# Kernel optimization log

Measured on AMD Instinct MI355X. Metric: run time of the kernel, lower is better.

Reference implementation:

```python
import jax, jax.numpy as jnp
import numpy as np

NUM_LOW, NUM_HIGH, DIM = 8192, 1024, 2048
EPS = 1e-10


def sparsemax(z):
    # z: [..., K]; Martins & Astudillo sparsemax along last axis.
    K = z.shape[-1]
    z_sorted = jnp.flip(jnp.sort(z, axis=-1), axis=-1)          # descending
    z_cum = jnp.cumsum(z_sorted, axis=-1)
    k = jnp.arange(1, K + 1, dtype=z.dtype)
    support = (1.0 + k * z_sorted) > z_cum                       # bool [..., K]
    k_sup = jnp.sum(support, axis=-1, keepdims=True)             # int [..., 1]
    tau = (jnp.take_along_axis(z_cum, k_sup - 1, axis=-1) - 1.0) / k_sup.astype(z.dtype)
    return jnp.maximum(z - tau, 0.0)


def normalize_rows(x, eps=EPS):
    return x / (jnp.sum(x, axis=1, keepdims=True) + eps)


def setup_inputs() -> dict:
    key = jax.random.key(0)
    k1, k2, k3, k4 = jax.random.split(key, 4)

    def xavier(k, shape):
        bound = float(np.sqrt(6.0 / (shape[0] + shape[1])))
        return jax.random.uniform(k, shape, jnp.float32, -bound, bound)

    return {
        "low_w": xavier(k1, (NUM_LOW, DIM)),    # low Concepts parameter
        "high_w": xavier(k2, (NUM_HIGH, DIM)),  # high Concepts parameter
        "Wq": xavier(k3, (DIM, DIM)),           # q_linear.weight (keep_head_dim, n_head=1)
        "Wk": xavier(k4, (DIM, DIM)),           # k_linear.weight
        "norm_low_concepts": 1,
        "norm_high_concepts": 1,
    }


def reference(low_w, high_w, Wq, Wk, norm_low_concepts, norm_high_concepts):
    # Concepts modules: return (possibly normalized) concepts + cosine similarity.
    low_normed = low_w / jnp.linalg.norm(low_w, axis=1, keepdims=True)
    low_concepts = low_normed if norm_low_concepts else low_w
    low_cos = low_normed @ low_normed.T                          # [NL, NL]

    high_normed = high_w / jnp.linalg.norm(high_w, axis=1, keepdims=True)
    high_concepts = high_normed if norm_high_concepts else high_w
    high_cos = high_normed @ high_normed.T                       # [NH, NH]

    # detach_low_concepts=True -> queries do not receive gradients
    low_q = jax.lax.stop_gradient(low_concepts)

    # ModifiedMultiHeadAttention (n_head=1, keep_head_dim -> d_head=DIM; eval mode,
    # so smooth_max is identity and sparsemax is deterministic).
    q = low_q @ Wq.T                                             # [NL, D]
    k = high_concepts @ Wk.T                                     # [NH, D]
    scale = 1.0 / jnp.sqrt(jnp.asarray(DIM, q.dtype))
    attn = sparsemax((q @ k.T) * scale)                          # [NL, NH]
    high_related_low = attn @ high_concepts                      # [NL, D]

    # output_high_concepts_type == "high_plus_low": add back aggregated low concepts
    aggregated_low = normalize_rows(attn.T) @ low_q              # [NH, D]
    output_high_concepts = high_related_low + attn @ aggregated_low  # [NL, D]

    return (low_concepts, low_cos, output_high_concepts, high_cos, attn)
```

## Files before the change

kernel.cpp:

```cpp
#include <hip/hip_runtime.h>
#include <hip/hip_bf16.h>
#include <stdint.h>

#define NL   8192
#define NHI  1024
#define DIMV 2048

typedef __attribute__((ext_vector_type(8))) short short8;
typedef __attribute__((ext_vector_type(4))) float f32x4;

__device__ __forceinline__ unsigned short f2bf(float x){
  unsigned u = __float_as_uint(x);
  u += 0x7FFFu + ((u >> 16) & 1u);
  return (unsigned short)(u >> 16);
}
__device__ __forceinline__ float bf2f(unsigned short b){
  return __uint_as_float(((unsigned)b) << 16);
}
__device__ __forceinline__ unsigned pack2bf(float a, float b){
  return (unsigned)f2bf(a) | ((unsigned)f2bf(b) << 16);
}

__device__ __forceinline__ void gload16(const void* g, void* l){
  __builtin_amdgcn_global_load_lds(
      (const __attribute__((address_space(1))) unsigned int*)g,
      (__attribute__((address_space(3))) unsigned int*)l, 16, 0, 0);
}

__global__ __launch_bounds__(256)
void prep_kernel(const float* __restrict__ low_w, const float* __restrict__ high_w,
                 const float* __restrict__ Wq, const float* __restrict__ Wk,
                 float* __restrict__ out_lowc, unsigned short* __restrict__ lowN,
                 unsigned short* __restrict__ highN,
                 unsigned short* __restrict__ WqB, unsigned short* __restrict__ WkB){
  int id = blockIdx.x;
  if(id < 9216){
    const float* W; float* oF; unsigned short* oB; int row;
    if(id < 8192){ W = low_w; oF = out_lowc; oB = lowN; row = id; }
    else         { W = high_w; oF = nullptr; oB = highN; row = id - 8192; }
    const float* r = W + (size_t)row * DIMV;
    int base = threadIdx.x * 8;
    float4 x0 = *(const float4*)(r + base);
    float4 x1 = *(const float4*)(r + base + 4);
    float ss = x0.x*x0.x + x0.y*x0.y + x0.z*x0.z + x0.w*x0.w
             + x1.x*x1.x + x1.y*x1.y + x1.z*x1.z + x1.w*x1.w;
    #pragma unroll
    for(int s = 1; s < 64; s <<= 1) ss += __shfl_xor(ss, s, 64);
    __shared__ float red[4];
    if((threadIdx.x & 63) == 0) red[threadIdx.x >> 6] = ss;
    __syncthreads();
    float tot = red[0] + red[1] + red[2] + red[3];
    float inv = 1.0f / sqrtf(tot);
    float y0=x0.x*inv, y1=x0.y*inv, y2=x0.z*inv, y3=x0.w*inv;
    float y4=x1.x*inv, y5=x1.y*inv, y6=x1.z*inv, y7=x1.w*inv;
    if(oF){
      float* o = oF + (size_t)row * DIMV + base;
      *(float4*)o       = make_float4(y0,y1,y2,y3);
      *(float4*)(o + 4) = make_float4(y4,y5,y6,y7);
    }
    uint4 u;
    u.x = pack2bf(y0,y1); u.y = pack2bf(y2,y3);
    u.z = pack2bf(y4,y5); u.w = pack2bf(y6,y7);
    *(uint4*)(oB + (size_t)row * DIMV + base) = u;
  } else {
    id -= 9216;
    const float* in; unsigned short* outp;
    if(id < 2048){ in = Wq; outp = WqB; } else { in = Wk; outp = WkB; id -= 2048; }
    size_t i = ((size_t)id * 256 + threadIdx.x) * 8;
    float4 x0 = *(const float4*)(in + i);
    float4 x1 = *(const float4*)(in + i + 4);
    uint4 u;
    u.x = pack2bf(x0.x,x0.y); u.y = pack2bf(x0.z,x0.w);
    u.z = pack2bf(x1.x,x1.y); u.w = pack2bf(x1.z,x1.w);
    *(uint4*)(outp + i) = u;
  }
}

template<int OUT_BF16, int MIRROR>
__global__ __launch_bounds__(256, 2)
void gemm_bt_kernel(const unsigned short* __restrict__ A,
                    const unsigned short* __restrict__ Bt,
                    float* __restrict__ Cf, unsigned short* __restrict__ Cb,
                    int M, int N, int K, float scale){
  __shared__ __align__(16) char smem[33792];
  unsigned short* sA = (unsigned short*)smem;
  unsigned short* sB = sA + 128 * 64;

  int tid = threadIdx.x, lane = tid & 63, wid = tid >> 6;
  int mBase, nBase;
  if(MIRROR){
    int nwg = gridDim.x;
    int id = blockIdx.x;
    int cpx = nwg >> 3;
    id = (id & 7) * cpx + (id >> 3);
    int bi = 0;
    while(((bi+1)*64 - (((bi+1)*bi) >> 1)) <= id) bi++;
    int off = bi*64 - ((bi*(bi-1)) >> 1);
    int bj = bi + (id - off);
    mBase = bi * 128; nBase = bj * 128;
  } else {
    int gx = gridDim.x, gy = gridDim.y;
    int nwg = gx * gy;
    int id = blockIdx.y * gx + blockIdx.x;
    if((nwg & 7) == 0){ int cpx = nwg >> 3; id = (id & 7) * cpx + (id >> 3); }
    mBase = (id / gx) * 128; nBase = (id % gx) * 128;
  }

  int chRow = lane >> 3;
  int chCol = (lane & 7) * 8;
  int wm = wid >> 1, wn = wid & 1;

  f32x4 acc[4][4];
  #pragma unroll
  for(int i=0;i<4;i++)
    #pragma unroll
    for(int j=0;j<4;j++) acc[i][j] = (f32x4){0.f,0.f,0.f,0.f};

  int kChunk = K / (int)gridDim.z;
  int kStart = kChunk * (int)blockIdx.z;
  if(!OUT_BF16) Cf += (size_t)blockIdx.z * M * N;

  for(int k0 = kStart; k0 < kStart + kChunk; k0 += 64){
    #pragma unroll
    for(int i = 0; i < 4; i++){
      int ch = wid * 4 + i;
      int arow = ch * 8 + chRow;
      gload16(A  + (size_t)(mBase + arow) * K + k0 + chCol, &sA[ch * 512]);
      gload16(Bt + (size_t)(nBase + arow) * K + k0 + chCol, &sB[ch * 512]);
    }
    __syncthreads();
    #pragma unroll
    for(int kk = 0; kk < 64; kk += 32){
      short8 a[4], b[4];
      int krd = kk + (lane >> 4) * 8;
      #pragma unroll
      for(int i = 0; i < 4; i++){
        int row = wm * 64 + i * 16 + (lane & 15);
        a[i] = *reinterpret_cast<const short8*>(&sA[row * 64 + krd]);
        int col = wn * 64 + i * 16 + (lane & 15);
        b[i] = *reinterpret_cast<const short8*>(&sB[col * 64 + krd]);
      }
      #pragma unroll
      for(int i = 0; i < 4; i++)
        #pragma unroll
        for(int j = 0; j < 4; j++)
          acc[i][j] = __builtin_amdgcn_mfma_f32_16x16x32_bf16(a[i], b[j], acc[i][j], 0, 0, 0);
    }
    __syncthreads();
  }

  #pragma unroll
  for(int i = 0; i < 4; i++){
    #pragma unroll
    for(int j = 0; j < 4; j++){
      int row = mBase + wm * 64 + i * 16 + (lane >> 4) * 4;
      int col = nBase + wn * 64 + j * 16 + (lane & 15);
      #pragma unroll
      for(int r = 0; r < 4; r++){
        float v = acc[i][j][r] * scale;
        size_t off = (size_t)(row + r) * N + col;
        if(OUT_BF16) Cb[off] = f2bf(v);
        else         Cf[off] = v;
      }
    }
  }

  if(MIRROR && mBase != nBase){
    float* T = (float*)(void*)(smem + wid * 8448);
    int ln15 = lane & 15, lh = lane >> 4;
    #pragma unroll
    for(int hh = 0; hh < 2; hh++){
      #pragma unroll
      for(int ii = 0; ii < 2; ii++){
        #pragma unroll
        for(int j = 0; j < 4; j++)
          #pragma unroll
          for(int r = 0; r < 4; r++)
            T[(j*16 + ln15)*33 + ii*16 + lh*4 + r] = acc[hh*2+ii][j][r] * scale;
      }
      asm volatile("s_waitcnt lgkmcnt(0)" ::: "memory");
      __builtin_amdgcn_sched_barrier(0);
      size_t gb = (size_t)(nBase + wn*64 + lane) * N + (mBase + wm*64 + hh*32);
      #pragma unroll
      for(int k4 = 0; k4 < 8; k4++){
        float4 v;
        v.x = T[lane*33 + k4*4 + 0];
        v.y = T[lane*33 + k4*4 + 1];
        v.z = T[lane*33 + k4*4 + 2];
        v.w = T[lane*33 + k4*4 + 3];
        *(float4*)(Cf + gb + k4*4) = v;
      }
      asm volatile("s_waitcnt lgkmcnt(0)" ::: "memory");
      __builtin_amdgcn_sched_barrier(0);
    }
  }
}

__global__ __launch_bounds__(256)
void combine2_kernel(const float* __restrict__ hcPart, float* __restrict__ out_highcos,
                     const float* __restrict__ kPart, unsigned short* __restrict__ kB){
  int id = blockIdx.x;
  if(id < 512){
    size_t i = ((size_t)id * 256 + threadIdx.x) * 8;
    float4 a0 = *(const float4*)(hcPart + i);
    float4 a1 = *(const float4*)(hcPart + i + 4);
    float4 b0 = *(const float4*)(hcPart + 1048576 + i);
    float4 b1 = *(const float4*)(hcPart + 1048576 + i + 4);
    *(float4*)(out_highcos + i)     = make_float4(a0.x+b0.x, a0.y+b0.y, a0.z+b0.z, a0.w+b0.w);
    *(float4*)(out_highcos + i + 4) = make_float4(a1.x+b1.x, a1.y+b1.y, a1.z+b1.z, a1.w+b1.w);
  } else {
    size_t i = ((size_t)(id - 512) * 256 + threadIdx.x) * 8;
    float4 a0 = *(const float4*)(kPart + i);
    float4 a1 = *(const float4*)(kPart + i + 4);
    float4 b0 = *(const float4*)(kPart + 2097152 + i);
    float4 b1 = *(const float4*)(kPart + 2097152 + i + 4);
    uint4 u;
    u.x = pack2bf(a0.x+b0.x, a0.y+b0.y); u.y = pack2bf(a0.z+b0.z, a0.w+b0.w);
    u.z = pack2bf(a1.x+b1.x, a1.y+b1.y); u.w = pack2bf(a1.z+b1.z, a1.w+b1.w);
    *(uint4*)(kB + i) = u;
  }
}

__global__ __launch_bounds__(256)
void sparsemax_kernel(float* __restrict__ S, unsigned short* __restrict__ attnBf){
  int wid = threadIdx.x >> 6, lane = threadIdx.x & 63;
  int row = blockIdx.x * 4 + wid;
  float* z = S + (size_t)row * NHI;
  float v[16];
  #pragma unroll
  for(int j = 0; j < 16; j++) v[j] = z[j * 64 + lane];
  float mx = v[0];
  #pragma unroll
  for(int j = 1; j < 16; j++) mx = fmaxf(mx, v[j]);
  #pragma unroll
  for(int s = 1; s < 64; s <<= 1) mx = fmaxf(mx, __shfl_xor(mx, s, 64));
  float lo = mx - 1.0f, hi = mx;
  for(int it = 0; it < 40; it++){
    float mid = 0.5f * (lo + hi);
    float sum = 0.f;
    #pragma unroll
    for(int j = 0; j < 16; j++) sum += fmaxf(v[j] - mid, 0.f);
    #pragma unroll
    for(int s = 1; s < 64; s <<= 1) sum += __shfl_xor(sum, s, 64);
    if(sum >= 1.0f) lo = mid; else hi = mid;
  }
  float cnt = 0.f, ssum = 0.f;
  #pragma unroll
  for(int j = 0; j < 16; j++){
    if(v[j] > lo){ cnt += 1.f; ssum += v[j]; }
  }
  #pragma unroll
  for(int s = 1; s < 64; s <<= 1){
    cnt  += __shfl_xor(cnt,  s, 64);
    ssum += __shfl_xor(ssum, s, 64);
  }
  float tau = (ssum - 1.0f) / cnt;
  #pragma unroll
  for(int j = 0; j < 16; j++){
    float a = fmaxf(v[j] - tau, 0.f);
    z[j * 64 + lane] = a;
    attnBf[(size_t)row * NHI + j * 64 + lane] = f2bf(a);
  }
}

__global__ __launch_bounds__(256)
void colsum_part_kernel(const float* __restrict__ attn, float* __restrict__ part){
  int chunk = blockIdx.x;
  int t = threadIdx.x;
  const float* p = attn + (size_t)chunk * 32 * NHI;
  float a0=0,a1=0,a2=0,a3=0;
  for(int r = 0; r < 32; r++){
    a0 += p[(size_t)r*NHI + t];
    a1 += p[(size_t)r*NHI + t + 256];
    a2 += p[(size_t)r*NHI + t + 512];
    a3 += p[(size_t)r*NHI + t + 768];
  }
  float* q = part + (size_t)chunk * NHI;
  q[t]=a0; q[t+256]=a1; q[t+512]=a2; q[t+768]=a3;
}
__global__ __launch_bounds__(256)
void colsum_final_kernel(const float* __restrict__ part, float* __restrict__ colsum){
  int c = blockIdx.x * 256 + threadIdx.x;
  float s = 0.f;
  for(int i = 0; i < 256; i++) s += part[(size_t)i * NHI + c];
  colsum[c] = s;
}

__global__ __launch_bounds__(256)
void transpose3_kernel(const unsigned short* __restrict__ attnB, unsigned short* __restrict__ attnT,
                       const unsigned short* __restrict__ lowN,  unsigned short* __restrict__ lowNT,
                       const unsigned short* __restrict__ highN, unsigned short* __restrict__ highNT){
  __shared__ unsigned short tile[64][65];
  int id = blockIdx.x;
  const unsigned short* in; unsigned short* out; int R, C, tx, ty;
  if(id < 2048){        in = attnB; out = attnT;  R = NL;  C = NHI;  tx = id & 15; ty = id >> 4; }
  else if(id < 6144){ id -= 2048;
                        in = lowN;  out = lowNT;  R = NL;  C = DIMV; tx = id & 31; ty = id >> 5; }
  else {              id -= 6144;
                        in = highN; out = highNT; R = NHI; C = DIMV; tx = id & 31; ty = id >> 5; }
  int c0 = tx * 64, r0 = ty * 64;
  int t = threadIdx.x;
  int ci = t & 63, r4 = t >> 6;
  #pragma unroll
  for(int k = 0; k < 16; k++){
    int r = k * 4 + r4;
    tile[r][ci] = in[(size_t)(r0 + r) * C + c0 + ci];
  }
  __syncthreads();
  #pragma unroll
  for(int k = 0; k < 16; k++){
    int cc = k * 4 + r4;
    out[(size_t)(c0 + cc) * R + r0 + ci] = tile[ci][cc];
  }
}

__global__ __launch_bounds__(256)
void mt_kernel(const unsigned short* __restrict__ highNT, const float* __restrict__ aggP,
               const float* __restrict__ colsum, unsigned short* __restrict__ Mt){
  int idx = blockIdx.x * 256 + threadIdx.x;
  int h = idx & 1023;
  float s = aggP[idx] + aggP[idx + 2097152] + aggP[idx + 4194304] + aggP[idx + 6291456];
  float val = bf2f(highNT[idx]) + s / (colsum[h] + 1e-10f);
  Mt[idx] = f2bf(val);
}

extern "C" void kernel_launch(void* const* d_in, const int* in_sizes, int n_in,
                              void* d_out, int out_size, void* d_ws, size_t ws_size,
                              hipStream_t stream){
  const float* low_w  = (const float*)d_in[0];
  const float* high_w = (const float*)d_in[1];
  const float* Wq     = (const float*)d_in[2];
  const float* Wk     = (const float*)d_in[3];
  float* out = (float*)d_out;

  char* ws = (char*)d_ws;
  unsigned short* lowN  = (unsigned short*)(ws);
  float*          aggP  = (float*)(ws);
  unsigned short* highN = (unsigned short*)(ws + 33554432);
  unsigned short* WqB   = (unsigned short*)(ws + 37748736);
  unsigned short* WkB   = (unsigned short*)(ws + 46137344);
  unsigned short* attnB = (unsigned short*)(ws + 37748736);
  unsigned short* qB    = (unsigned short*)(ws + 54525952);
  unsigned short* lowNT = qB;
  unsigned short* kB    = (unsigned short*)(ws + 88080384);
  float*          part  = (float*)(ws + 88080384);
  float*          colsum= (float*)(ws + 88080384 + 1048576);
  unsigned short* attnT = (unsigned short*)(ws + 92274688);
  float*          kPart = (float*)(ws + 92274688);
  unsigned short* Mt    = (unsigned short*)(ws + 109051904);
  unsigned short* highNT= (unsigned short*)(ws + 113246208);
  float*          hcPart= (float*)(ws + 109051904);

  float* out_lowc    = out;
  float* out_lowcos  = out + 16777216;
  float* out_high    = out + 83886080;
  float* out_highcos = out + 100663296;
  float* out_attn    = out + 101711872;

  const float scl = 1.0f / sqrtf((float)DIMV);

  prep_kernel<<<13312, 256, 0, stream>>>(low_w, high_w, Wq, Wk,
                                         out_lowc, lowN, highN, WqB, WkB);
  gemm_bt_kernel<0,1><<<2080, 256, 0, stream>>>(lowN, lowN, out_lowcos, nullptr,
                                                NL, NL, DIMV, 1.0f);
  gemm_bt_kernel<0,0><<<dim3(8,8,2), 256, 0, stream>>>(highN, highN, hcPart, nullptr,
                                                       NHI, NHI, DIMV, 1.0f);
  gemm_bt_kernel<0,0><<<dim3(16,8,2), 256, 0, stream>>>(highN, WkB, kPart, nullptr,
                                                        NHI, DIMV, DIMV, 1.0f);
  combine2_kernel<<<1536, 256, 0, stream>>>(hcPart, out_highcos, kPart, kB);
  gemm_bt_kernel<1,0><<<dim3(16,64), 256, 0, stream>>>(lowN, WqB, nullptr, qB,
                                                       NL, DIMV, DIMV, 1.0f);
  gemm_bt_kernel<0,0><<<dim3(8,64), 256, 0, stream>>>(qB, kB, out_attn, nullptr,
                                                      NL, NHI, DIMV, scl);
  sparsemax_kernel<<<NL/4, 256, 0, stream>>>(out_attn, attnB);
  colsum_part_kernel<<<256, 256, 0, stream>>>(out_attn, part);
  colsum_final_kernel<<<4, 256, 0, stream>>>(part, colsum);
  transpose3_kernel<<<6656, 256, 0, stream>>>(attnB, attnT, lowN, lowNT, highN, highNT);
  gemm_bt_kernel<0,0><<<dim3(8,16,4), 256, 0, stream>>>(lowNT, attnT, aggP, nullptr,
                                                        DIMV, NHI, NL, 1.0f);
  mt_kernel<<<8192, 256, 0, stream>>>(highNT, aggP, colsum, Mt);
  gemm_bt_kernel<0,0><<<dim3(16,64), 256, 0, stream>>>(attnB, Mt, out_high, nullptr,
                                                       NL, DIMV, NHI, 1.0f);
}
```

Before: 657.5 us.

## Move symmetric cosine mirroring into separate transpose kernel and halve split-K

Drops the in-GEMM mirrored write of the off-diagonal lower-triangle tiles for the low cosine matrix. A standalone mirror_kernel instead reads each upper tile back and writes it transposed through a shared-memory tile. This shrinks the GEMM's shared memory and epilogue, at the cost of an extra read pass over the upper half of the output. Separately, the aggregation GEMM's split-K goes from 4 to 2 partitions, and mt_kernel sums two partials instead of four.

```diff
diff --git a/kernel.cpp b/kernel.cpp
--- a/kernel.cpp
+++ b/kernel.cpp
@@ -82,7 +82,7 @@
                     const unsigned short* __restrict__ Bt,
                     float* __restrict__ Cf, unsigned short* __restrict__ Cb,
                     int M, int N, int K, float scale){
-  __shared__ __align__(16) char smem[33792];
+  __shared__ __align__(16) char smem[32768];
   unsigned short* sA = (unsigned short*)smem;
   unsigned short* sB = sA + 128 * 64;
 
@@ -164,34 +164,35 @@
       }
     }
   }
-
-  if(MIRROR && mBase != nBase){
-    float* T = (float*)(void*)(smem + wid * 8448);
-    int ln15 = lane & 15, lh = lane >> 4;
-    #pragma unroll
-    for(int hh = 0; hh < 2; hh++){
-      #pragma unroll
-      for(int ii = 0; ii < 2; ii++){
-        #pragma unroll
-        for(int j = 0; j < 4; j++)
-          #pragma unroll
-          for(int r = 0; r < 4; r++)
-            T[(j*16 + ln15)*33 + ii*16 + lh*4 + r] = acc[hh*2+ii][j][r] * scale;
-      }
-      asm volatile("s_waitcnt lgkmcnt(0)" ::: "memory");
-      __builtin_amdgcn_sched_barrier(0);
-      size_t gb = (size_t)(nBase + wn*64 + lane) * N + (mBase + wm*64 + hh*32);
-      #pragma unroll
-      for(int k4 = 0; k4 < 8; k4++){
-        float4 v;
-        v.x = T[lane*33 + k4*4 + 0];
-        v.y = T[lane*33 + k4*4 + 1];
-        v.z = T[lane*33 + k4*4 + 2];
-        v.w = T[lane*33 + k4*4 + 3];
-        *(float4*)(Cf + gb + k4*4) = v;
-      }
-      asm volatile("s_waitcnt lgkmcnt(0)" ::: "memory");
-      __builtin_amdgcn_sched_barrier(0);
+}
+
+__global__ __launch_bounds__(256)
+void mirror_kernel(float* __restrict__ C){
+  int id = blockIdx.x;
+  int cpx = 2016 >> 3;
+  id = (id & 7) * cpx + (id >> 3);
+  int bi = 0;
+  while(((bi+1)*63 - (((bi+1)*bi) >> 1)) <= id) bi++;
+  int off = bi*63 - ((bi*(bi-1)) >> 1);
+  int bj = bi + 1 + (id - off);
+  __shared__ float tile[64][65];
+  int t = threadIdx.x;
+  int ci = t & 63, r4 = t >> 6;
+  #pragma unroll
+  for(int q = 0; q < 4; q++){
+    int qr = q >> 1, qc = q & 1;
+    int r0 = bi*128 + qr*64, c0 = bj*128 + qc*64;
+    __syncthreads();
+    #pragma unroll
+    for(int k = 0; k < 16; k++){
+      int r = k*4 + r4;
+      tile[r][ci] = C[(size_t)(r0 + r)*NL + c0 + ci];
+    }
+    __syncthreads();
+    #pragma unroll
+    for(int k = 0; k < 16; k++){
+      int cc = k*4 + r4;
+      C[(size_t)(c0 + cc)*NL + r0 + ci] = tile[ci][cc];
     }
   }
 }
@@ -319,7 +320,7 @@
                const float* __restrict__ colsum, unsigned short* __restrict__ Mt){
   int idx = blockIdx.x * 256 + threadIdx.x;
   int h = idx & 1023;
-  float s = aggP[idx] + aggP[idx + 2097152] + aggP[idx + 4194304] + aggP[idx + 6291456];
+  float s = aggP[idx] + aggP[idx + 2097152];
   float val = bf2f(highNT[idx]) + s / (colsum[h] + 1e-10f);
   Mt[idx] = f2bf(val);
 }
@@ -363,6 +364,7 @@
                                          out_lowc, lowN, highN, WqB, WkB);
   gemm_bt_kernel<0,1><<<2080, 256, 0, stream>>>(lowN, lowN, out_lowcos, nullptr,
                                                 NL, NL, DIMV, 1.0f);
+  mirror_kernel<<<2016, 256, 0, stream>>>(out_lowcos);
   gemm_bt_kernel<0,0><<<dim3(8,8,2), 256, 0, stream>>>(highN, highN, hcPart, nullptr,
                                                        NHI, NHI, DIMV, 1.0f);
   gemm_bt_kernel<0,0><<<dim3(16,8,2), 256, 0, stream>>>(highN, WkB, kPart, nullptr,
@@ -376,7 +378,7 @@
   colsum_part_kernel<<<256, 256, 0, stream>>>(out_attn, part);
   colsum_final_kernel<<<4, 256, 0, stream>>>(part, colsum);
   transpose3_kernel<<<6656, 256, 0, stream>>>(attnB, attnT, lowN, lowNT, highN, highNT);
-  gemm_bt_kernel<0,0><<<dim3(8,16,4), 256, 0, stream>>>(lowNT, attnT, aggP, nullptr,
+  gemm_bt_kernel<0,0><<<dim3(8,16,2), 256, 0, stream>>>(lowNT, attnT, aggP, nullptr,
                                                         DIMV, NHI, NL, 1.0f);
   mt_kernel<<<8192, 256, 0, stream>>>(highNT, aggP, colsum, Mt);
   gemm_bt_kernel<0,0><<<dim3(16,64), 256, 0, stream>>>(attnB, Mt, out_high, nullptr,
```

After: 663.3 us. About the same (+0.9%).

## Supertile symmetric Gram schedule, block-wide mirror transpose, halve split-K for aggregation

Applied to the files above, without the earlier changes.

The symmetric low-cosine GEMM now walks upper-triangle tiles in 4x4 supertile groups, so neighbouring workgroups share A/B row panels in cache. The mirrored transpose write is redone as a block-wide staging through one 64x65 shared tile per quadrant, with __syncthreads between quadrants. This cuts shared memory to 32 KB but adds barriers. The aggregation GEMM's split-K drops from 4 to 2, so mt_kernel reads fewer partials, at the cost of less parallelism in that GEMM.

```diff
diff --git a/kernel.cpp b/kernel.cpp
--- a/kernel.cpp
+++ b/kernel.cpp
@@ -82,21 +82,30 @@
                     const unsigned short* __restrict__ Bt,
                     float* __restrict__ Cf, unsigned short* __restrict__ Cb,
                     int M, int N, int K, float scale){
-  __shared__ __align__(16) char smem[33792];
+  __shared__ __align__(16) char smem[32768];
   unsigned short* sA = (unsigned short*)smem;
   unsigned short* sB = sA + 128 * 64;
 
   int tid = threadIdx.x, lane = tid & 63, wid = tid >> 6;
   int mBase, nBase;
   if(MIRROR){
-    int nwg = gridDim.x;
-    int id = blockIdx.x;
-    int cpx = nwg >> 3;
-    id = (id & 7) * cpx + (id >> 3);
-    int bi = 0;
-    while(((bi+1)*64 - (((bi+1)*bi) >> 1)) <= id) bi++;
-    int off = bi*64 - ((bi*(bi-1)) >> 1);
-    int bj = bi + (id - off);
+    int orig = blockIdx.x;
+    int id = (orig & 7) * 260 + (orig >> 3);
+    int Si = 0, rem = id;
+    for(;;){ int rl = 10 + 16*(15 - Si); if(rem < rl) break; rem -= rl; Si++; }
+    int bi, bj;
+    if(rem < 10){
+      int ti = 0;
+      while((ti+1)*4 - (((ti+1)*ti) >> 1) <= rem) ti++;
+      int off = ti*4 - ((ti*(ti-1)) >> 1);
+      int tj = ti + (rem - off);
+      bi = Si*4 + ti; bj = Si*4 + tj;
+    } else {
+      int r2 = rem - 10;
+      int Sj = Si + 1 + (r2 >> 4);
+      int t = r2 & 15;
+      bi = Si*4 + (t >> 2); bj = Sj*4 + (t & 3);
+    }
     mBase = bi * 128; nBase = bj * 128;
   } else {
     int gx = gridDim.x, gy = gridDim.y;
@@ -166,32 +175,35 @@
   }
 
   if(MIRROR && mBase != nBase){
-    float* T = (float*)(void*)(smem + wid * 8448);
-    int ln15 = lane & 15, lh = lane >> 4;
-    #pragma unroll
-    for(int hh = 0; hh < 2; hh++){
+    float* tf = (float*)smem;
+    #pragma unroll
+    for(int rq = 0; rq < 4; rq++){
+      int qm = rq >> 1, qn = rq & 1;
+      __syncthreads();
+      if(wm == qm && wn == qn){
+        #pragma unroll
+        for(int i = 0; i < 4; i++)
+          #pragma unroll
+          for(int j = 0; j < 4; j++){
+            int rl = i * 16 + (lane >> 4) * 4;
+            int cl = j * 16 + (lane & 15);
+            #pragma unroll
+            for(int r = 0; r < 4; r++)
+              tf[(rl + r) * 65 + cl] = acc[i][j][r] * scale;
+          }
+      }
+      __syncthreads();
+      int mr = tid >> 2, seg = tid & 3;
+      size_t obase = (size_t)(nBase + qn * 64 + mr) * N + mBase + qm * 64 + seg * 16;
       #pragma unroll
-      for(int ii = 0; ii < 2; ii++){
-        #pragma unroll
-        for(int j = 0; j < 4; j++)
-          #pragma unroll
-          for(int r = 0; r < 4; r++)
-            T[(j*16 + ln15)*33 + ii*16 + lh*4 + r] = acc[hh*2+ii][j][r] * scale;
+      for(int k4 = 0; k4 < 4; k4++){
+        float4 v;
+        v.x = tf[(seg * 16 + k4 * 4 + 0) * 65 + mr];
+        v.y = tf[(seg * 16 + k4 * 4 + 1) * 65 + mr];
+        v.z = tf[(seg * 16 + k4 * 4 + 2) * 65 + mr];
+        v.w = tf[(seg * 16 + k4 * 4 + 3) * 65 + mr];
+        *(float4*)(Cf + obase + k4 * 4) = v;
       }
-      asm volatile("s_waitcnt lgkmcnt(0)" ::: "memory");
-      __builtin_amdgcn_sched_barrier(0);
-      size_t gb = (size_t)(nBase + wn*64 + lane) * N + (mBase + wm*64 + hh*32);
-      #pragma unroll
-      for(int k4 = 0; k4 < 8; k4++){
-        float4 v;
-        v.x = T[lane*33 + k4*4 + 0];
-        v.y = T[lane*33 + k4*4 + 1];
-        v.z = T[lane*33 + k4*4 + 2];
-        v.w = T[lane*33 + k4*4 + 3];
-        *(float4*)(Cf + gb + k4*4) = v;
-      }
-      asm volatile("s_waitcnt lgkmcnt(0)" ::: "memory");
-      __builtin_amdgcn_sched_barrier(0);
     }
   }
 }
@@ -319,7 +331,7 @@
                const float* __restrict__ colsum, unsigned short* __restrict__ Mt){
   int idx = blockIdx.x * 256 + threadIdx.x;
   int h = idx & 1023;
-  float s = aggP[idx] + aggP[idx + 2097152] + aggP[idx + 4194304] + aggP[idx + 6291456];
+  float s = aggP[idx] + aggP[idx + 2097152];
   float val = bf2f(highNT[idx]) + s / (colsum[h] + 1e-10f);
   Mt[idx] = f2bf(val);
 }
@@ -376,7 +388,7 @@
   colsum_part_kernel<<<256, 256, 0, stream>>>(out_attn, part);
   colsum_final_kernel<<<4, 256, 0, stream>>>(part, colsum);
   transpose3_kernel<<<6656, 256, 0, stream>>>(attnB, attnT, lowN, lowNT, highN, highNT);
-  gemm_bt_kernel<0,0><<<dim3(8,16,4), 256, 0, stream>>>(lowNT, attnT, aggP, nullptr,
+  gemm_bt_kernel<0,0><<<dim3(8,16,2), 256, 0, stream>>>(lowNT, attnT, aggP, nullptr,
                                                         DIMV, NHI, NL, 1.0f);
   mt_kernel<<<8192, 256, 0, stream>>>(highNT, aggP, colsum, Mt);
   gemm_bt_kernel<0,0><<<dim3(16,64), 256, 0, stream>>>(attnB, Mt, out_high, nullptr,
```

New measurement: 628.7 us. 4.4% less time.
